# Performance work log

Measured on AMD Instinct MI355X. Metric: run time of the kernel, lower is better.

## Reference

```python
import jax, jax.numpy as jnp
import numpy as np

MARGIN = 0.1
SEMIHARD = True


def setup_inputs() -> dict:
    key = jax.random.key(0)
    k1, k2 = jax.random.split(key)
    N, D = 512, 128
    embeddings = jax.random.normal(k1, (N, D), dtype=jnp.float32)
    labels = jax.random.randint(k2, (N,), 0, 64, dtype=jnp.int64)
    return {"embeddings": embeddings, "labels": labels}


def _triplet_mask(labels):
    # mask[a, p, n] True iff a,p,n distinct, labels[a]==labels[p], labels[a]!=labels[n]
    n = labels.shape[0]
    ine = ~jnp.eye(n, dtype=bool)                       # [N, N] i != j
    distinct = ine[:, :, None] & ine[:, None, :] & ine[None, :, :]
    leq = labels[None, :] == labels[:, None]            # [N, N] label equality
    valid = leq[:, :, None] & ~leq[:, None, :]
    return distinct & valid


def reference(embeddings, labels):
    # L2-normalize rows, cosine similarity matrix
    norms = jnp.linalg.norm(embeddings, ord=2, axis=1, keepdims=True)
    e = embeddings / norms
    all_sim = e @ e.T                                   # [N, N]
    mask = _triplet_mask(labels).astype(all_sim.dtype)  # [N, N, N]
    # loss[a,p,n] = relu(-sim[a,p] + sim[a,n] + margin) * mask
    anc_pos = all_sim[:, :, None]                       # [N, N, 1]
    anc_neg = all_sim[:, None, :]                       # [N, 1, N]
    loss = jax.nn.relu(anc_neg - anc_pos + MARGIN) * mask
    if SEMIHARD:
        num_active = jnp.sum((loss > 1e-16).astype(loss.dtype))
        return jnp.sum(loss) / (num_active + 1e-16)
    else:
        return jnp.sum(loss) / jnp.sum(mask)
```

## Files before the change

### kernel.cpp

```cpp
#include <hip/hip_runtime.h>
#include <math.h>

#define MARGIN 0.1f
#define NN 512
#define DD 128
#define NT 256
#define AB 2
#define TROWS 64
#define NTILES (NN / TROWS)
#define NBLK (NN / AB)
#define MAXPOS 256

__global__ __launch_bounds__(NT) void triplet_partial_kernel(
        const float* __restrict__ emb, const int* __restrict__ labels,
        double* __restrict__ part_sum, int* __restrict__ part_cnt) {
    __shared__ int   lab[NN];
    __shared__ __align__(16) float ea[AB][DD];
    __shared__ __align__(16) float tile[TROWS * DD];
    __shared__ float simr[AB][NN];
    __shared__ int   pos[AB][MAXPOS];
    __shared__ int   npos[AB];
    __shared__ double red_s[NT / 64];
    __shared__ int    red_c[NT / 64];

    const int b  = blockIdx.x;
    const int t  = threadIdx.x;
    const int a0 = b * AB;
    const int jj = t >> 2;
    const int ks = t & 3;

    for (int j = t; j < NN; j += NT) lab[j] = labels[j];
    {
        int ai = t >> 7;
        int k  = t & 127;
        ea[ai][k] = emb[(size_t)(a0 + ai) * DD + k];
    }
    if (t < AB) npos[t] = 0;
    __syncthreads();

    float w0[32], w1[32];
    #pragma unroll
    for (int i = 0; i < 32; ++i) {
        w0[i] = ea[0][ks * 32 + i];
        w1[i] = ea[1][ks * 32 + i];
    }

    float nsq0 = 0.f, nsq1 = 0.f;
    #pragma unroll
    for (int i = 0; i < 32; ++i) {
        nsq0 += w0[i] * w0[i];
        nsq1 += w1[i] * w1[i];
    }
    nsq0 += __shfl_xor(nsq0, 1, 64); nsq0 += __shfl_xor(nsq0, 2, 64);
    nsq1 += __shfl_xor(nsq1, 1, 64); nsq1 += __shfl_xor(nsq1, 2, 64);
    const float inva0 = 1.0f / sqrtf(nsq0);
    const float inva1 = 1.0f / sqrtf(nsq1);

    const float4* __restrict__ emb4 = reinterpret_cast<const float4*>(emb);
    float4* tile4 = reinterpret_cast<float4*>(tile);

    for (int tl = 0; tl < NTILES; ++tl) {
        const int rbase = tl * TROWS;
        __syncthreads();
        #pragma unroll
        for (int it = 0; it < 8; ++it) {
            int c   = t + NT * it;
            int row = c >> 5;
            int c4  = c & 31;
            float4 v = emb4[(size_t)(rbase + row) * 32 + c4];
            tile4[row * 32 + (c4 ^ (row & 7))] = v;
        }
        __syncthreads();

        float d0 = 0.f, d1 = 0.f, nsq = 0.f;
        #pragma unroll
        for (int i2 = 0; i2 < 8; ++i2) {
            float4 v = tile4[jj * 32 + ((ks * 8 + i2) ^ (jj & 7))];
            int ib = i2 * 4;
            d0  += v.x * w0[ib] + v.y * w0[ib + 1] + v.z * w0[ib + 2] + v.w * w0[ib + 3];
            d1  += v.x * w1[ib] + v.y * w1[ib + 1] + v.z * w1[ib + 2] + v.w * w1[ib + 3];
            nsq += v.x * v.x + v.y * v.y + v.z * v.z + v.w * v.w;
        }
        d0  += __shfl_xor(d0, 1, 64);  d0  += __shfl_xor(d0, 2, 64);
        d1  += __shfl_xor(d1, 1, 64);  d1  += __shfl_xor(d1, 2, 64);
        nsq += __shfl_xor(nsq, 1, 64); nsq += __shfl_xor(nsq, 2, 64);
        if (ks == 0) {
            float rn = 1.0f / sqrtf(nsq);
            int j = rbase + jj;
            simr[0][j] = d0 * inva0 * rn;
            simr[1][j] = d1 * inva1 * rn;
        }
    }
    __syncthreads();

    for (int j = t; j < NN; j += NT) {
        #pragma unroll
        for (int ai = 0; ai < AB; ++ai) {
            if (j != a0 + ai && lab[j] == lab[a0 + ai]) {
                int idx = atomicAdd(&npos[ai], 1);
                if (idx < MAXPOS) pos[ai][idx] = j;
            }
        }
    }
    __syncthreads();

    double lsum = 0.0;
    int    lcnt = 0;
    #pragma unroll
    for (int ai = 0; ai < AB; ++ai) {
        const int la = lab[a0 + ai];
        const int np = min(npos[ai], MAXPOS);
        for (int pi = 0; pi < np; ++pi) {
            const float sap = simr[ai][pos[ai][pi]];
            for (int n = t; n < NN; n += NT) {
                if (lab[n] != la) {
                    float d = simr[ai][n] - sap + MARGIN;
                    if (d > 0.f)    lsum += (double)d;
                    if (d > 1e-16f) lcnt += 1;
                }
            }
        }
    }

    for (int off = 32; off > 0; off >>= 1) {
        lsum += __shfl_down(lsum, off, 64);
        lcnt += __shfl_down(lcnt, off, 64);
    }
    const int wid = t >> 6, lane = t & 63;
    if (lane == 0) { red_s[wid] = lsum; red_c[wid] = lcnt; }
    __syncthreads();
    if (t == 0) {
        double s = 0.0; int c = 0;
        for (int w = 0; w < NT / 64; ++w) { s += red_s[w]; c += red_c[w]; }
        part_sum[b] = s;
        part_cnt[b] = c;
    }
}

__global__ __launch_bounds__(NBLK) void finalize_kernel(
        const double* __restrict__ part_sum, const int* __restrict__ part_cnt,
        float* __restrict__ out) {
    __shared__ double rs[NBLK / 64];
    __shared__ int    rc[NBLK / 64];
    const int t = threadIdx.x;
    double s = part_sum[t];
    int    c = part_cnt[t];
    for (int off = 32; off > 0; off >>= 1) {
        s += __shfl_down(s, off, 64);
        c += __shfl_down(c, off, 64);
    }
    const int wid = t >> 6, lane = t & 63;
    if (lane == 0) { rs[wid] = s; rc[wid] = c; }
    __syncthreads();
    if (t == 0) {
        double S = 0.0; int C = 0;
        for (int w = 0; w < NBLK / 64; ++w) { S += rs[w]; C += rc[w]; }
        out[0] = (float)(S / ((double)C + 1e-16));
    }
}

extern "C" void kernel_launch(void* const* d_in, const int* in_sizes, int n_in,
                              void* d_out, int out_size, void* d_ws, size_t ws_size,
                              hipStream_t stream) {
    const float* emb  = (const float*)d_in[0];
    const int* labels = (const int*)d_in[1];

    double* part_sum = (double*)d_ws;
    int*    part_cnt = (int*)((char*)d_ws + NBLK * sizeof(double));
    float*  out      = (float*)d_out;

    triplet_partial_kernel<<<NBLK, NT, 0, stream>>>(emb, labels, part_sum, part_cnt);
    finalize_kernel<<<1, NBLK, 0, stream>>>(part_sum, part_cnt, out);
}
```

Measured before the change: 74.79 us.

## Read embedding rows directly from global memory and double block threads

Drops the shared-memory tile staging and its per-tile barriers. Each 4-thread group now loads its own row with coalesced float4 global reads and computes the dot products in registers. The block grows to 512 threads so each thread owns one negative index, and the loss loop hoists that index's similarity and label out of the positive loop. In exchange the kernel uses more registers per thread and relies on L2 for the repeated embedding reads across blocks.

```diff
diff --git a/kernel.cpp b/kernel.cpp
--- a/kernel.cpp
+++ b/kernel.cpp
@@ -4,10 +4,10 @@
 #define MARGIN 0.1f
 #define NN 512
 #define DD 128
-#define NT 256
+#define NT 512
 #define AB 2
-#define TROWS 64
-#define NTILES (NN / TROWS)
+#define GROUPS (NT / 4)
+#define NTILES (NN / GROUPS)
 #define NBLK (NN / AB)
 #define MAXPOS 256
 
@@ -16,7 +16,6 @@
         double* __restrict__ part_sum, int* __restrict__ part_cnt) {
     __shared__ int   lab[NN];
     __shared__ __align__(16) float ea[AB][DD];
-    __shared__ __align__(16) float tile[TROWS * DD];
     __shared__ float simr[AB][NN];
     __shared__ int   pos[AB][MAXPOS];
     __shared__ int   npos[AB];
@@ -26,74 +25,79 @@
     const int b  = blockIdx.x;
     const int t  = threadIdx.x;
     const int a0 = b * AB;
-    const int jj = t >> 2;
+    const int g  = t >> 2;
     const int ks = t & 3;
 
-    for (int j = t; j < NN; j += NT) lab[j] = labels[j];
-    {
-        int ai = t >> 7;
-        int k  = t & 127;
-        ea[ai][k] = emb[(size_t)(a0 + ai) * DD + k];
+    lab[t] = labels[t];
+    if (t < AB * DD) {
+        ea[t >> 7][t & 127] = emb[(size_t)(a0 + (t >> 7)) * DD + (t & 127)];
     }
     if (t < AB) npos[t] = 0;
     __syncthreads();
 
-    float w0[32], w1[32];
+    const float4* __restrict__ emb4 = reinterpret_cast<const float4*>(emb);
+    const float4* ea4 = reinterpret_cast<const float4*>(&ea[0][0]);
+
+    float4 w0[8], w1[8];
     #pragma unroll
-    for (int i = 0; i < 32; ++i) {
-        w0[i] = ea[0][ks * 32 + i];
-        w1[i] = ea[1][ks * 32 + i];
+    for (int i2 = 0; i2 < 8; ++i2) {
+        w0[i2] = ea4[i2 * 4 + ks];
+        w1[i2] = ea4[32 + i2 * 4 + ks];
     }
 
     float nsq0 = 0.f, nsq1 = 0.f;
     #pragma unroll
-    for (int i = 0; i < 32; ++i) {
-        nsq0 += w0[i] * w0[i];
-        nsq1 += w1[i] * w1[i];
+    for (int i2 = 0; i2 < 8; ++i2) {
+        nsq0 += w0[i2].x * w0[i2].x + w0[i2].y * w0[i2].y
+              + w0[i2].z * w0[i2].z + w0[i2].w * w0[i2].w;
+        nsq1 += w1[i2].x * w1[i2].x + w1[i2].y * w1[i2].y
+              + w1[i2].z * w1[i2].z + w1[i2].w * w1[i2].w;
     }
     nsq0 += __shfl_xor(nsq0, 1, 64); nsq0 += __shfl_xor(nsq0, 2, 64);
     nsq1 += __shfl_xor(nsq1, 1, 64); nsq1 += __shfl_xor(nsq1, 2, 64);
     const float inva0 = 1.0f / sqrtf(nsq0);
     const float inva1 = 1.0f / sqrtf(nsq1);
 
-    const float4* __restrict__ emb4 = reinterpret_cast<const float4*>(emb);
-    float4* tile4 = reinterpret_cast<float4*>(tile);
+    #pragma unroll 2
+    for (int tl = 0; tl < NTILES; ++tl) {
+        const int r = tl * GROUPS + g;
+        float4 v[8];
+        #pragma unroll
+        for (int i2 = 0; i2 < 8; ++i2)
+            v[i2] = emb4[(size_t)r * 32 + i2 * 4 + ks];
 
-    for (int tl = 0; tl < NTILES; ++tl) {
-        const int rbase = tl * TROWS;
-        __syncthreads();
+        float d0a = 0.f, d0b = 0.f, d1a = 0.f, d1b = 0.f, na = 0.f, nb = 0.f;
         #pragma unroll
-        for (int it = 0; it < 8; ++it) {
-            int c   = t + NT * it;
-            int row = c >> 5;
-            int c4  = c & 31;
-            float4 v = emb4[(size_t)(rbase + row) * 32 + c4];
-            tile4[row * 32 + (c4 ^ (row & 7))] = v;
+        for (int i2 = 0; i2 < 8; i2 += 2) {
+            d0a += v[i2].x * w0[i2].x + v[i2].y * w0[i2].y
+                 + v[i2].z * w0[i2].z + v[i2].w * w0[i2].w;
+            d1a += v[i2].x * w1[i2].x + v[i2].y * w1[i2].y
+                 + v[i2].z * w1[i2].z + v[i2].w * w1[i2].w;
+            na  += v[i2].x * v[i2].x + v[i2].y * v[i2].y
+                 + v[i2].z * v[i2].z + v[i2].w * v[i2].w;
+            const int j2 = i2 + 1;
+            d0b += v[j2].x * w0[j2].x + v[j2].y * w0[j2].y
+                 + v[j2].z * w0[j2].z + v[j2].w * w0[j2].w;
+            d1b += v[j2].x * w1[j2].x + v[j2].y * w1[j2].y
+                 + v[j2].z * w1[j2].z + v[j2].w * w1[j2].w;
+            nb  += v[j2].x * v[j2].x + v[j2].y * v[j2].y
+                 + v[j2].z * v[j2].z + v[j2].w * v[j2].w;
         }
-        __syncthreads();
+        float d0 = d0a + d0b, d1 = d1a + d1b, nsq = na + nb;
 
-        float d0 = 0.f, d1 = 0.f, nsq = 0.f;
-        #pragma unroll
-        for (int i2 = 0; i2 < 8; ++i2) {
-            float4 v = tile4[jj * 32 + ((ks * 8 + i2) ^ (jj & 7))];
-            int ib = i2 * 4;
-            d0  += v.x * w0[ib] + v.y * w0[ib + 1] + v.z * w0[ib + 2] + v.w * w0[ib + 3];
-            d1  += v.x * w1[ib] + v.y * w1[ib + 1] + v.z * w1[ib + 2] + v.w * w1[ib + 3];
-            nsq += v.x * v.x + v.y * v.y + v.z * v.z + v.w * v.w;
-        }
         d0  += __shfl_xor(d0, 1, 64);  d0  += __shfl_xor(d0, 2, 64);
         d1  += __shfl_xor(d1, 1, 64);  d1  += __shfl_xor(d1, 2, 64);
         nsq += __shfl_xor(nsq, 1, 64); nsq += __shfl_xor(nsq, 2, 64);
         if (ks == 0) {
-            float rn = 1.0f / sqrtf(nsq);
-            int j = rbase + jj;
-            simr[0][j] = d0 * inva0 * rn;
-            simr[1][j] = d1 * inva1 * rn;
+            const float rn = 1.0f / sqrtf(nsq);
+            simr[0][r] = d0 * inva0 * rn;
+            simr[1][r] = d1 * inva1 * rn;
         }
     }
     __syncthreads();
 
-    for (int j = t; j < NN; j += NT) {
+    {
+        const int j = t;
         #pragma unroll
         for (int ai = 0; ai < AB; ++ai) {
             if (j != a0 + ai && lab[j] == lab[a0 + ai]) {
@@ -104,20 +108,32 @@
     }
     __syncthreads();
 
+    const int   myLab = lab[t];
+    const float sn0   = simr[0][t];
+    const float sn1   = simr[1][t];
     double lsum = 0.0;
     int    lcnt = 0;
-    #pragma unroll
-    for (int ai = 0; ai < AB; ++ai) {
-        const int la = lab[a0 + ai];
-        const int np = min(npos[ai], MAXPOS);
-        for (int pi = 0; pi < np; ++pi) {
-            const float sap = simr[ai][pos[ai][pi]];
-            for (int n = t; n < NN; n += NT) {
-                if (lab[n] != la) {
-                    float d = simr[ai][n] - sap + MARGIN;
-                    if (d > 0.f)    lsum += (double)d;
-                    if (d > 1e-16f) lcnt += 1;
-                }
+    {
+        const int la = lab[a0];
+        if (myLab != la) {
+            const int np = min(npos[0], MAXPOS);
+            for (int pi = 0; pi < np; ++pi) {
+                const float sap = simr[0][pos[0][pi]];
+                const float d = sn0 - sap + MARGIN;
+                if (d > 0.f)    lsum += (double)d;
+                if (d > 1e-16f) lcnt += 1;
+            }
+        }
+    }
+    {
+        const int la = lab[a0 + 1];
+        if (myLab != la) {
+            const int np = min(npos[1], MAXPOS);
+            for (int pi = 0; pi < np; ++pi) {
+                const float sap = simr[1][pos[1][pi]];
+                const float d = sn1 - sap + MARGIN;
+                if (d > 0.f)    lsum += (double)d;
+                if (d > 1e-16f) lcnt += 1;
             }
         }
     }
```

Result: faster. 63.29 us (-15.4%).
